# Kernel tuning notes

Hardware: AMD Instinct MI355X
Metric: run time of the kernel (lower is better)

The kernel has to match this reference:

```python
import jax, jax.numpy as jnp
import numpy as np


def setup_inputs() -> dict:
    key = jax.random.key(0)
    kK, kV, kQ = jax.random.split(key, 3)
    B, D, S = 4, 64, 4096
    K = jax.random.normal(kK, (B, D, S), dtype=jnp.float32)
    V = jax.random.normal(kV, (B, D, S), dtype=jnp.float32)
    Q = jax.random.normal(kQ, (B, D, S), dtype=jnp.float32)
    return {"K": K, "V": V, "Q": Q}


def reference(K, V, Q):
    # K,V: [B, D, Sk], Q: [B, D, Sq]
    d = Q.shape[1]
    # A[b,k,q] = sum_d K[b,d,k] * Q[b,d,q] / sqrt(d)
    A = jnp.einsum("bdk,bdq->bkq", K, Q) / jnp.sqrt(jnp.asarray(d, Q.dtype))
    A = jax.nn.softmax(A, axis=1)  # normalize over keys (dim 1), matching F.softmax(A, 1)
    # R[b,d,q] = sum_k V[b,d,k] * A[b,k,q]
    R = jnp.einsum("bdk,bkq->bdq", V, A)
    return jnp.concatenate((R, Q), axis=1)  # [B, 2D, Sq]
```

## Files before the change

kernel.cpp:

```cpp
#include <hip/hip_runtime.h>
#include <hip/hip_bf16.h>

#define S_LEN 4096
#define D_DIM 64
#define QB 64
#define KB 32
#define NT (S_LEN / KB)
#define TILE_E 4096

typedef __attribute__((ext_vector_type(8)))  short bf16x8;
typedef __attribute__((ext_vector_type(16))) float f32x16;
typedef unsigned int u32;

#define Z16 {0.f,0.f,0.f,0.f,0.f,0.f,0.f,0.f,0.f,0.f,0.f,0.f,0.f,0.f,0.f,0.f}

union bpack8 { __hip_bfloat16 h[8]; bf16x8 v; };
union ppack  { u32 w[4]; bf16x8 v; };

static __device__ __forceinline__ float fexp2(float x) {
    return __builtin_amdgcn_exp2f(x);
}
static __device__ __forceinline__ u32 cvtpk(float lo, float hi) {
    u32 r;
    asm("v_cvt_pk_bf16_f32 %0, %1, %2" : "=v"(r) : "v"(lo), "v"(hi));
    return r;
}
static __device__ __forceinline__ void plswap(u32 &a, u32 &b) {
    asm("v_permlane32_swap_b32 %0, %1" : "+v"(a), "+v"(b));
}

struct pfrag { ppack p0, p1; };
static __device__ __forceinline__ pfrag packP(const f32x16& s) {
    u32 A = cvtpk(s[0],  s[1]),  Bw = cvtpk(s[2],  s[3]);
    u32 C = cvtpk(s[4],  s[5]),  Dw = cvtpk(s[6],  s[7]);
    u32 E = cvtpk(s[8],  s[9]),  F  = cvtpk(s[10], s[11]);
    u32 G = cvtpk(s[12], s[13]), H  = cvtpk(s[14], s[15]);
    plswap(A, C); plswap(Bw, Dw); plswap(E, G); plswap(F, H);
    pfrag r;
    r.p0.w[0] = A; r.p0.w[1] = Bw; r.p0.w[2] = C; r.p0.w[3] = Dw;
    r.p1.w[0] = E; r.p1.w[1] = F;  r.p1.w[2] = G; r.p1.w[3] = H;
    return r;
}
static __device__ __forceinline__ float treesum(const f32x16& s) {
    float a0 = (s[0] + s[1])   + (s[2] + s[3]);
    float a1 = (s[4] + s[5])   + (s[6] + s[7]);
    float a2 = (s[8] + s[9])   + (s[10] + s[11]);
    float a3 = (s[12] + s[13]) + (s[14] + s[15]);
    return (a0 + a1) + (a2 + a3);
}

#define GLD16(gp, lp) __builtin_amdgcn_global_load_lds( \
    (const __attribute__((address_space(1))) u32*)(const void*)(gp), \
    (__attribute__((address_space(3))) u32*)(void*)(lp), 16, 0, 0)

#define QSCALE 0.18033688011112042f

__global__ __launch_bounds__(256)
void prep_all(const float* __restrict__ K, const float* __restrict__ V,
              const float* __restrict__ Q,
              __hip_bfloat16* __restrict__ KVbf, __hip_bfloat16* __restrict__ Qbf,
              float* __restrict__ out)
{
    const int b = blockIdx.y, x = blockIdx.x, z = blockIdx.z;
    const int t = threadIdx.x;

    if (z == 0) {
        const int key = t & 31, dg = t >> 5;
        const float* src = K + ((size_t)b * D_DIM + dg * 8) * S_LEN + x * KB + key;
        bpack8 u;
        #pragma unroll
        for (int e = 0; e < 8; ++e)
            u.h[e] = __float2bfloat16(src[(size_t)e * S_LEN]);
        *(bf16x8*)&KVbf[((size_t)b * NT + x) * TILE_E + t * 8] = u.v;
    } else if (z == 1) {
        const int kg = t >> 6, d = t & 63;
        const float* p = V + ((size_t)b * D_DIM + d) * S_LEN + x * KB + kg * 8;
        float4 a = *(const float4*)p, c = *(const float4*)(p + 4);
        bpack8 u;
        u.h[0] = __float2bfloat16(a.x); u.h[1] = __float2bfloat16(a.y);
        u.h[2] = __float2bfloat16(a.z); u.h[3] = __float2bfloat16(a.w);
        u.h[4] = __float2bfloat16(c.x); u.h[5] = __float2bfloat16(c.y);
        u.h[6] = __float2bfloat16(c.z); u.h[7] = __float2bfloat16(c.w);
        *(bf16x8*)&KVbf[((size_t)b * NT + x) * TILE_E + 2048 + t * 8] = u.v;
    } else {
        const int q = x * 32 + (t & 31), dg = t >> 5;
        const float* src = Q + ((size_t)b * D_DIM + dg * 8) * S_LEN + q;
        float r[8];
        #pragma unroll
        for (int e = 0; e < 8; ++e) r[e] = src[(size_t)e * S_LEN];
        float* o = out + ((size_t)b * 2 * D_DIM + D_DIM + dg * 8) * S_LEN + q;
        #pragma unroll
        for (int e = 0; e < 8; ++e) o[(size_t)e * S_LEN] = r[e];
        bpack8 u;
        #pragma unroll
        for (int e = 0; e < 8; ++e) u.h[e] = __float2bfloat16(r[e] * QSCALE);
        *(bf16x8*)&Qbf[((size_t)b * S_LEN + q) * D_DIM + dg * 8] = u.v;
    }
}

__global__ __launch_bounds__(512, 2)
void attn_fwd(const __hip_bfloat16* __restrict__ KVbf,
              const __hip_bfloat16* __restrict__ Qbf,
              float* __restrict__ out)
{
    const int b  = blockIdx.y;
    const int q0 = blockIdx.x * QB;
    const int t  = threadIdx.x;
    const int lane = t & 63;
    const int w    = t >> 6;
    const int l5   = lane & 31;
    const int h    = lane >> 5;

    __shared__ __align__(16) char Ls[131072];
    char* myL = Ls + w * 16384;

    const int WT = NT / 8;
    const __hip_bfloat16* kvb = KVbf + ((size_t)b * NT + w * WT) * TILE_E;

    const __hip_bfloat16* qrowA = Qbf + ((size_t)b * S_LEN + q0 + l5) * D_DIM;
    const __hip_bfloat16* qrowB = qrowA + 32 * D_DIM;
    bf16x8 qfA[4], qfB[4];
    #pragma unroll
    for (int j = 0; j < 4; ++j) {
        qfA[j] = *(const bf16x8*)&qrowA[(2 * j + h) * 8];
        qfB[j] = *(const bf16x8*)&qrowB[(2 * j + h) * 8];
    }

    #pragma unroll
    for (int i = 0; i < 8; ++i)
        GLD16(kvb + i * 512 + lane * 8, myL + i * 1024);
    asm volatile("s_waitcnt vmcnt(0)" ::: "memory");
    __builtin_amdgcn_sched_barrier(0);

    float lsumA = 0.f, lsumB = 0.f;
    f32x16 accA[2] = {Z16, Z16}, accB[2] = {Z16, Z16};
    int cur = 0;

    for (int it = 0; it < WT; ++it) {
        if (it + 1 < WT) {
            const __hip_bfloat16* nx = kvb + (size_t)(it + 1) * TILE_E;
            #pragma unroll
            for (int i = 0; i < 8; ++i)
                GLD16(nx + i * 512 + lane * 8, myL + (cur ^ 1) * 8192 + i * 1024);
        }
        const char* Lk = myL + cur * 8192;
        const char* Lv = Lk + 4096;

        bf16x8 kf[4];
        #pragma unroll
        for (int j = 0; j < 4; ++j)
            kf[j] = *(const bf16x8*)(Lk + ((2 * j + h) * 32 + l5) * 16);

        f32x16 sA = Z16, sB = Z16;
        __builtin_amdgcn_s_setprio(1);
        #pragma unroll
        for (int j = 0; j < 4; ++j) {
            sA = __builtin_amdgcn_mfma_f32_32x32x16_bf16(kf[j], qfA[j], sA, 0, 0, 0);
            sB = __builtin_amdgcn_mfma_f32_32x32x16_bf16(kf[j], qfB[j], sB, 0, 0, 0);
        }
        __builtin_amdgcn_s_setprio(0);

        bf16x8 vf[4];
        #pragma unroll
        for (int j = 0; j < 2; ++j)
            #pragma unroll
            for (int dt = 0; dt < 2; ++dt)
                vf[2 * j + dt] = *(const bf16x8*)(Lv + ((2 * j + h) * 64 + dt * 32 + l5) * 16);

        #pragma unroll
        for (int r = 0; r < 16; ++r) sA[r] = fexp2(sA[r]);
        #pragma unroll
        for (int r = 0; r < 16; ++r) sB[r] = fexp2(sB[r]);
        lsumA += treesum(sA);
        lsumB += treesum(sB);

        pfrag pA = packP(sA), pB = packP(sB);

        __builtin_amdgcn_s_setprio(1);
        #pragma unroll
        for (int j = 0; j < 2; ++j)
            #pragma unroll
            for (int dt = 0; dt < 2; ++dt) {
                const bf16x8 vv = vf[2 * j + dt];
                const ppack& pa = j ? pA.p1 : pA.p0;
                const ppack& pb = j ? pB.p1 : pB.p0;
                accA[dt] = __builtin_amdgcn_mfma_f32_32x32x16_bf16(vv, pa.v, accA[dt], 0, 0, 0);
                accB[dt] = __builtin_amdgcn_mfma_f32_32x32x16_bf16(vv, pb.v, accB[dt], 0, 0, 0);
            }
        __builtin_amdgcn_s_setprio(0);

        asm volatile("s_waitcnt vmcnt(0)" ::: "memory");
        __builtin_amdgcn_sched_barrier(0);
        cur ^= 1;
    }

    lsumA += __shfl_xor(lsumA, 32);
    lsumB += __shfl_xor(lsumB, 32);

    float* LF = (float*)Ls;
    __syncthreads();
    if (h == 0) {
        LF[w * 64 + l5]      = lsumA;
        LF[w * 64 + 32 + l5] = lsumB;
    }
    __syncthreads();
    const int qp = t & 63;
    float den = 0.f;
    #pragma unroll
    for (int w2 = 0; w2 < 8; ++w2) den += LF[w2 * 64 + qp];
    const float inv = 1.f / den;
    __syncthreads();

    #pragma unroll
    for (int dt = 0; dt < 2; ++dt)
        #pragma unroll
        for (int r = 0; r < 16; ++r) {
            int d = dt * 32 + (r & 3) + 8 * (r >> 2) + 4 * h;
            LF[w * 2048 + d * 32 + l5]         = accA[dt][r];
            LF[16384 + w * 2048 + d * 32 + l5] = accB[dt][r];
        }
    __syncthreads();

    const int dgrp = t >> 6;
    const int slab = (qp < 32) ? 0 : 16384;
    const int qs   = qp & 31;
    float* op = out + (size_t)b * 2 * D_DIM * S_LEN + q0 + qp;
    #pragma unroll
    for (int dd = 0; dd < 8; ++dd) {
        int d = dgrp * 8 + dd;
        float sum = 0.f;
        #pragma unroll
        for (int w2 = 0; w2 < 8; ++w2)
            sum += LF[slab + w2 * 2048 + d * 32 + qs];
        op[(size_t)d * S_LEN] = sum * inv;
    }
}

extern "C" void kernel_launch(void* const* d_in, const int* in_sizes, int n_in,
                              void* d_out, int out_size, void* d_ws, size_t ws_size,
                              hipStream_t stream) {
    const float* K = (const float*)d_in[0];
    const float* V = (const float*)d_in[1];
    const float* Q = (const float*)d_in[2];
    float* out = (float*)d_out;

    const int B = in_sizes[0] / (D_DIM * S_LEN);
    const size_t kvE = (size_t)B * NT * TILE_E;

    __hip_bfloat16* KVbf = (__hip_bfloat16*)d_ws;
    __hip_bfloat16* Qbf  = KVbf + kvE;

    prep_all<<<dim3(NT, B, 3), dim3(256), 0, stream>>>(K, V, Q, KVbf, Qbf, out);

    attn_fwd<<<dim3(S_LEN / QB, B), dim3(512), 0, stream>>>(KVbf, Qbf, out);
}
```

Baseline: 35.56 us.

## Fuse Q conversion and Q passthrough copy into attention kernel

The bf16 Q conversion and the copy of Q into the second half of the output move out of the prep kernel and into the attention kernel. Each block loads its fp32 Q tile, scales it and transposes it through shared memory, then packs it to bf16 in registers. At the end the block writes the raw Q rows to the output. This removes the Qbf workspace round trip and shrinks the prep launch, at the cost of extra syncs and LDS traffic at attention start. The V conversion thread mapping is also changed so that neighbouring threads read contiguous keys of the same row, improving coalescing while keeping the same packed layout.

```diff
diff --git a/kernel.cpp b/kernel.cpp
--- a/kernel.cpp
+++ b/kernel.cpp
@@ -56,10 +56,8 @@
 #define QSCALE 0.18033688011112042f
 
 __global__ __launch_bounds__(256)
-void prep_all(const float* __restrict__ K, const float* __restrict__ V,
-              const float* __restrict__ Q,
-              __hip_bfloat16* __restrict__ KVbf, __hip_bfloat16* __restrict__ Qbf,
-              float* __restrict__ out)
+void prep_kv(const float* __restrict__ K, const float* __restrict__ V,
+             __hip_bfloat16* __restrict__ KVbf)
 {
     const int b = blockIdx.y, x = blockIdx.x, z = blockIdx.z;
     const int t = threadIdx.x;
@@ -72,8 +70,8 @@
         for (int e = 0; e < 8; ++e)
             u.h[e] = __float2bfloat16(src[(size_t)e * S_LEN]);
         *(bf16x8*)&KVbf[((size_t)b * NT + x) * TILE_E + t * 8] = u.v;
-    } else if (z == 1) {
-        const int kg = t >> 6, d = t & 63;
+    } else {
+        const int d = t >> 2, kg = t & 3;
         const float* p = V + ((size_t)b * D_DIM + d) * S_LEN + x * KB + kg * 8;
         float4 a = *(const float4*)p, c = *(const float4*)(p + 4);
         bpack8 u;
@@ -81,26 +79,13 @@
         u.h[2] = __float2bfloat16(a.z); u.h[3] = __float2bfloat16(a.w);
         u.h[4] = __float2bfloat16(c.x); u.h[5] = __float2bfloat16(c.y);
         u.h[6] = __float2bfloat16(c.z); u.h[7] = __float2bfloat16(c.w);
-        *(bf16x8*)&KVbf[((size_t)b * NT + x) * TILE_E + 2048 + t * 8] = u.v;
-    } else {
-        const int q = x * 32 + (t & 31), dg = t >> 5;
-        const float* src = Q + ((size_t)b * D_DIM + dg * 8) * S_LEN + q;
-        float r[8];
-        #pragma unroll
-        for (int e = 0; e < 8; ++e) r[e] = src[(size_t)e * S_LEN];
-        float* o = out + ((size_t)b * 2 * D_DIM + D_DIM + dg * 8) * S_LEN + q;
-        #pragma unroll
-        for (int e = 0; e < 8; ++e) o[(size_t)e * S_LEN] = r[e];
-        bpack8 u;
-        #pragma unroll
-        for (int e = 0; e < 8; ++e) u.h[e] = __float2bfloat16(r[e] * QSCALE);
-        *(bf16x8*)&Qbf[((size_t)b * S_LEN + q) * D_DIM + dg * 8] = u.v;
+        *(bf16x8*)&KVbf[((size_t)b * NT + x) * TILE_E + 2048 + (kg * 64 + d) * 8] = u.v;
     }
 }
 
 __global__ __launch_bounds__(512, 2)
 void attn_fwd(const __hip_bfloat16* __restrict__ KVbf,
-              const __hip_bfloat16* __restrict__ Qbf,
+              const float* __restrict__ Qg,
               float* __restrict__ out)
 {
     const int b  = blockIdx.y;
@@ -116,14 +101,39 @@
 
     const int WT = NT / 8;
     const __hip_bfloat16* kvb = KVbf + ((size_t)b * NT + w * WT) * TILE_E;
-
-    const __hip_bfloat16* qrowA = Qbf + ((size_t)b * S_LEN + q0 + l5) * D_DIM;
-    const __hip_bfloat16* qrowB = qrowA + 32 * D_DIM;
+    const float* Qblk = Qg + (size_t)b * D_DIM * S_LEN + q0;
+
+    {
+        float* QF = (float*)Ls;
+        #pragma unroll
+        for (int i = 0; i < 8; ++i) {
+            int d = i * 8 + w;
+            QF[d * 65 + lane] = Qblk[(size_t)d * S_LEN + lane] * QSCALE;
+        }
+        __syncthreads();
+    }
     bf16x8 qfA[4], qfB[4];
-    #pragma unroll
-    for (int j = 0; j < 4; ++j) {
-        qfA[j] = *(const bf16x8*)&qrowA[(2 * j + h) * 8];
-        qfB[j] = *(const bf16x8*)&qrowB[(2 * j + h) * 8];
+    {
+        const float* QF = (const float*)Ls;
+        #pragma unroll
+        for (int j = 0; j < 4; ++j) {
+            float a[8], bq[8];
+            #pragma unroll
+            for (int e = 0; e < 8; ++e) {
+                int dabs = (2 * j + h) * 8 + e;
+                a[e]  = QF[dabs * 65 + l5];
+                bq[e] = QF[dabs * 65 + 32 + l5];
+            }
+            ppack pa, pb;
+            #pragma unroll
+            for (int k2 = 0; k2 < 4; ++k2) {
+                pa.w[k2] = cvtpk(a[2 * k2],  a[2 * k2 + 1]);
+                pb.w[k2] = cvtpk(bq[2 * k2], bq[2 * k2 + 1]);
+            }
+            qfA[j] = pa.v;
+            qfB[j] = pb.v;
+        }
+        __syncthreads();
     }
 
     #pragma unroll
@@ -234,6 +244,15 @@
             sum += LF[slab + w2 * 2048 + d * 32 + qs];
         op[(size_t)d * S_LEN] = sum * inv;
     }
+
+    {
+        float* oq = out + ((size_t)b * 2 * D_DIM + D_DIM) * S_LEN + q0;
+        #pragma unroll
+        for (int i = 0; i < 8; ++i) {
+            int d = i * 8 + w;
+            oq[(size_t)d * S_LEN + lane] = Qblk[(size_t)d * S_LEN + lane];
+        }
+    }
 }
 
 extern "C" void kernel_launch(void* const* d_in, const int* in_sizes, int n_in,
@@ -245,12 +264,9 @@
     float* out = (float*)d_out;
 
     const int B = in_sizes[0] / (D_DIM * S_LEN);
-    const size_t kvE = (size_t)B * NT * TILE_E;
-
     __hip_bfloat16* KVbf = (__hip_bfloat16*)d_ws;
-    __hip_bfloat16* Qbf  = KVbf + kvE;
-
-    prep_all<<<dim3(NT, B, 3), dim3(256), 0, stream>>>(K, V, Q, KVbf, Qbf, out);
-
-    attn_fwd<<<dim3(S_LEN / QB, B), dim3(512), 0, stream>>>(KVbf, Qbf, out);
-}
+
+    prep_kv<<<dim3(NT, B, 2), dim3(256), 0, stream>>>(K, V, KVbf);
+
+    attn_fwd<<<dim3(S_LEN / QB, B), dim3(512), 0, stream>>>(KVbf, Q, out);
+}
```

After: 34.42 us. 1.03x faster.
